# Optimization experiments

Hardware: AMD Instinct MI355X
Metric: run time of the kernel (lower is better)

## Reference

```python
import jax, jax.numpy as jnp
import numpy as np

N_ENT, N_REL, DIM, N_BASES = 100000, 474, 200, 100
N_EDGES, N_TRIPLES = 500000, 200000


def setup_inputs() -> dict:
    key = jax.random.key(0)
    ks = jax.random.split(key, 12)
    s = np.sqrt(2.0 / (1 + 0.01 ** 2))  # kaiming-ish scale (exact init irrelevant for correctness baseline)
    return {
        "entity_embeds": jax.random.normal(ks[0], (N_ENT, DIM), jnp.float32) * 0.05,
        "bases": jax.random.normal(ks[1], (N_BASES, DIM), jnp.float32) * 0.05,
        "coefficients": jax.random.normal(ks[2], (N_REL, N_BASES), jnp.float32) * 0.05,
        "w1": jax.random.normal(ks[3], (3, DIM, DIM), jnp.float32) * (s / np.sqrt(DIM)),
        "rw1": jax.random.normal(ks[4], (DIM, DIM), jnp.float32) * (s / np.sqrt(DIM)),
        "w2": jax.random.normal(ks[5], (3, DIM, DIM), jnp.float32) * (s / np.sqrt(DIM)),
        "rw2": jax.random.normal(ks[6], (DIM, DIM), jnp.float32) * (s / np.sqrt(DIM)),
        "ent_ids": jnp.arange(N_ENT, dtype=jnp.int32),
        "edge_index": jax.random.randint(ks[7], (2, N_EDGES), 0, N_ENT, jnp.int32),
        "edge_type": jax.random.randint(ks[8], (N_EDGES,), 0, N_REL, jnp.int32),
        "y": jax.random.randint(ks[9], (N_EDGES,), 0, 3, jnp.int32),
        "triples": jax.random.randint(ks[10], (N_TRIPLES, 3), 0, N_REL, jnp.int32),
    }


def _compgcn_layer(x, r, W, RW, edge_index, edge_type, y, n_nodes):
    # message: x_j + r[edge_type], then per-edge-direction linear transform W[y]
    msgs = x[edge_index[0]] + r[edge_type]            # [E, d]
    t = jnp.einsum('ed,kdf->kef', msgs, W)            # [3, E, d] (avoids [E,d,d] gather)
    sel = jnp.where(y[:, None] == 0, t[0], jnp.where(y[:, None] == 1, t[1], t[2]))  # [E, d]
    agg = jax.ops.segment_sum(sel, edge_index[1], num_segments=n_nodes)  # aggr='add'
    return jnp.tanh(agg), r @ RW


def reference(entity_embeds, bases, coefficients, w1, rw1, w2, rw2,
              ent_ids, edge_index, edge_type, y, triples):
    # encode (eval mode: dropout is identity)
    x = entity_embeds[ent_ids]
    r = coefficients @ bases                          # [num_relations, d]
    n_nodes = x.shape[0]
    x, r = _compgcn_layer(x, r, w1, rw1, edge_index, edge_type, y, n_nodes)
    x, r = _compgcn_layer(x, r, w2, rw2, edge_index, edge_type, y, n_nodes)
    # L2 normalize (torch eps=1e-12)
    x = x / jnp.maximum(jnp.linalg.norm(x, axis=1, keepdims=True), 1e-12)
    # decode: TransE-style L1 distance, sigmoid
    h = x[triples[:, 0]]
    rel = r[triples[:, 1]]
    t = x[triples[:, 2]]
    scores = jnp.sum(jnp.abs(h + rel - t), axis=1)    # norm p=1
    return jax.nn.sigmoid(scores)
```

## Files before the change

kernel.cpp:

```cpp
#include <hip/hip_runtime.h>
#include <math.h>


#define NENT     100000
#define NREL     474
#define DIM      200
#define NBASES   100
#define NEDGES   500000
#define NTRIPLES 200000

#define CHUNK    50000
#define NCHUNKS  2
#define SD       608
#define KD       608
#define NPAD     224
#define NTILW    7

#define OFF_R1    0UL
#define OFF_R2    380928UL
#define OFF_R3    761856UL
#define OFF_R1B   1142784UL
#define OFF_R2B   1335296UL
#define OFF_DEG   1527808UL
#define OFF_CUR   1929216UL
#define OFF_CSR   2330624UL
#define OFF_BSUM  2732032UL
#define OFF_BOFF  2736128UL
#define OFF_CSRC  2740224UL
#define OFF_CRY   4743168UL
#define OFF_WT1   6746112UL
#define OFF_WT2   7020544UL
#define OFF_ENTB  7294976UL
#define OFF_X1B   47296512UL
#define OFF_SBUF  87298048UL
#define OFF_X2    148099072UL

typedef __attribute__((ext_vector_type(8))) short bf16x8;
typedef __attribute__((ext_vector_type(4))) float f32x4;

__device__ inline unsigned short f2bf(float f) {
    unsigned u = __float_as_uint(f);
    return (unsigned short)((u + 0x7FFFu + ((u >> 16) & 1u)) >> 16);
}
__device__ inline float bf2f(unsigned short s) {
    return __uint_as_float(((unsigned)s) << 16);
}

__global__ __launch_bounds__(256) void k_small_gemm(
    const float* __restrict__ A, const float* __restrict__ B,
    float* __restrict__ C, int M, int K, int N)
{
    int tid = blockIdx.x * blockDim.x + threadIdx.x;
    if (tid >= M * N) return;
    int row = tid / N, col = tid - row * N;
    const float* a = A + (long)row * K;
    float acc = 0.f;
    int k = 0;
    for (; k + 4 <= K; k += 4) {
        acc = fmaf(a[k + 0], B[(k + 0) * N + col], acc);
        acc = fmaf(a[k + 1], B[(k + 1) * N + col], acc);
        acc = fmaf(a[k + 2], B[(k + 2) * N + col], acc);
        acc = fmaf(a[k + 3], B[(k + 3) * N + col], acc);
    }
    for (; k < K; ++k) acc = fmaf(a[k], B[k * N + col], acc);
    C[tid] = acc;
}

__global__ __launch_bounds__(256) void k_rb(const float* __restrict__ in,
                                            unsigned short* __restrict__ out, int n)
{
    int i = blockIdx.x * 256 + threadIdx.x;
    if (i < n) out[i] = f2bf(in[i]);
}

__global__ __launch_bounds__(256) void k_wt(const float* __restrict__ W,
                                            unsigned short* __restrict__ Wt)
{
    int i = blockIdx.x * 256 + threadIdx.x;
    if (i >= NPAD * KD) return;
    int c = i / KD, k = i - c * KD;
    float v = (c < 200 && k < 600) ? W[k * 200 + c] : 0.f;
    Wt[i] = f2bf(v);
}

__global__ __launch_bounds__(256) void k_entb(const float4* __restrict__ ent,
                                              const int* __restrict__ ids,
                                              ushort4* __restrict__ out)
{
    int i = blockIdx.x * 256 + threadIdx.x;
    if (i >= NENT * 50) return;
    int node = i / 50, j = i - node * 50;
    float4 v = ent[(long)ids[node] * 50 + j];
    ushort4 o;
    o.x = f2bf(v.x); o.y = f2bf(v.y); o.z = f2bf(v.z); o.w = f2bf(v.w);
    out[i] = o;
}

__global__ __launch_bounds__(256) void k_hist(const int* __restrict__ ei, int* __restrict__ deg)
{
    int e = blockIdx.x * blockDim.x + threadIdx.x;
    if (e >= NEDGES) return;
    atomicAdd(&deg[ei[NEDGES + e]], 1);
}

__global__ __launch_bounds__(256) void k_scanA(
    const int* __restrict__ deg, int* __restrict__ out, int* __restrict__ bsum)
{
    __shared__ int sd[256];
    int t = threadIdx.x, b = blockIdx.x;
    int base = b * 1024 + t * 4;
    int v0 = (base + 0 < NENT) ? deg[base + 0] : 0;
    int v1 = (base + 1 < NENT) ? deg[base + 1] : 0;
    int v2 = (base + 2 < NENT) ? deg[base + 2] : 0;
    int v3 = (base + 3 < NENT) ? deg[base + 3] : 0;
    int s = v0 + v1 + v2 + v3;
    sd[t] = s; __syncthreads();
    for (int off = 1; off < 256; off <<= 1) {
        int x = (t >= off) ? sd[t - off] : 0;
        __syncthreads();
        sd[t] += x;
        __syncthreads();
    }
    int excl = sd[t] - s;
    if (base + 0 < NENT) out[base + 0] = excl;
    if (base + 1 < NENT) out[base + 1] = excl + v0;
    if (base + 2 < NENT) out[base + 2] = excl + v0 + v1;
    if (base + 3 < NENT) out[base + 3] = excl + v0 + v1 + v2;
    if (t == 255) bsum[b] = sd[255];
}

__global__ __launch_bounds__(128) void k_scanB(
    const int* __restrict__ bsum, int* __restrict__ boff, int nb)
{
    __shared__ int sd[128];
    int t = threadIdx.x;
    int s = (t < nb) ? bsum[t] : 0;
    sd[t] = s; __syncthreads();
    for (int off = 1; off < 128; off <<= 1) {
        int x = (t >= off) ? sd[t - off] : 0;
        __syncthreads();
        sd[t] += x;
        __syncthreads();
    }
    if (t < nb) boff[t] = sd[t] - s;
}

__global__ __launch_bounds__(256) void k_scanC(int* __restrict__ csr, const int* __restrict__ boff)
{
    int t = threadIdx.x, b = blockIdx.x;
    int base = b * 1024 + t * 4;
    int add = boff[b];
    #pragma unroll
    for (int i = 0; i < 4; ++i)
        if (base + i < NENT) csr[base + i] += add;
    if (b == 0 && t == 0) csr[NENT] = NEDGES;
}

__global__ __launch_bounds__(256) void k_scatter(
    const int* __restrict__ ei, const int* __restrict__ et, const int* __restrict__ y,
    const int* __restrict__ csr, int* __restrict__ cur,
    int* __restrict__ csrc, int* __restrict__ cry)
{
    int e = blockIdx.x * blockDim.x + threadIdx.x;
    if (e >= NEDGES) return;
    int dst = ei[NEDGES + e];
    int pos = csr[dst] + atomicAdd(&cur[dst], 1);
    csrc[pos] = ei[e];
    cry[pos]  = et[e] | (y[e] << 16);
}

__global__ __launch_bounds__(256) void k_accum(
    const unsigned short* __restrict__ xb,
    const unsigned short* __restrict__ rb,
    const int* __restrict__ csr, const int* __restrict__ csrc, const int* __restrict__ cry,
    unsigned short* __restrict__ S, int nodeBase)
{
    int wv   = (blockIdx.x * blockDim.x + threadIdx.x) >> 6;
    int lane = threadIdx.x & 63;
    unsigned short* srow = S + (long)wv * SD;
    if (lane >= 50) {
        if (lane == 50) {
            uint4 z; z.x = z.y = z.z = z.w = 0u;
            *(uint4*)(srow + 600) = z;
        }
        return;
    }
    int v = nodeBase + wv;
    int start = csr[v], end = csr[v + 1];
    float4 a0 = {0,0,0,0}, a1 = {0,0,0,0}, a2 = {0,0,0,0};
    for (int e = start; e < end; ++e) {
        int src = csrc[e];
        int ry  = cry[e];
        int rel = ry & 0xFFFF;
        int k   = ry >> 16;
        ushort4 xv = *(const ushort4*)(xb + (long)src * 200 + lane * 4);
        ushort4 rv = *(const ushort4*)(rb + (long)rel * 200 + lane * 4);
        float mx = bf2f(xv.x) + bf2f(rv.x), my = bf2f(xv.y) + bf2f(rv.y);
        float mz = bf2f(xv.z) + bf2f(rv.z), mw = bf2f(xv.w) + bf2f(rv.w);
        if (k == 0)      { a0.x += mx; a0.y += my; a0.z += mz; a0.w += mw; }
        else if (k == 1) { a1.x += mx; a1.y += my; a1.z += mz; a1.w += mw; }
        else             { a2.x += mx; a2.y += my; a2.z += mz; a2.w += mw; }
    }
    ushort4 o;
    o.x = f2bf(a0.x); o.y = f2bf(a0.y); o.z = f2bf(a0.z); o.w = f2bf(a0.w);
    *(ushort4*)(srow +   0 + lane * 4) = o;
    o.x = f2bf(a1.x); o.y = f2bf(a1.y); o.z = f2bf(a1.z); o.w = f2bf(a1.w);
    *(ushort4*)(srow + 200 + lane * 4) = o;
    o.x = f2bf(a2.x); o.y = f2bf(a2.y); o.z = f2bf(a2.z); o.w = f2bf(a2.w);
    *(ushort4*)(srow + 400 + lane * 4) = o;
}

template<int OUTBF>
__global__ __launch_bounds__(256) void k_gemm_mfma(
    const unsigned short* __restrict__ S, const unsigned short* __restrict__ Wt,
    void* __restrict__ Xout, int nrows, int rowBase)
{
    int wid  = threadIdx.x >> 6;
    int lane = threadIdx.x & 63;
    int l15  = lane & 15;
    int l4   = lane >> 4;
    int row0 = blockIdx.x * 32 + (wid & 1) * 16;
    int nt0  = (wid >> 1) * NTILW;
    int ra = row0 + l15; if (ra >= nrows) ra = nrows - 1;
    const unsigned short* pa = S  + (long)ra * SD + l4 * 8;
    const unsigned short* pw = Wt + (long)(nt0 * 16 + l15) * KD + l4 * 8;

    f32x4 acc[NTILW] = {};
    for (int kt = 0; kt < 19; ++kt) {
        bf16x8 a = *(const bf16x8*)(pa + kt * 32);
        #pragma unroll
        for (int nt = 0; nt < NTILW; ++nt) {
            bf16x8 b = *(const bf16x8*)(pw + nt * 16 * KD + kt * 32);
            acc[nt] = __builtin_amdgcn_mfma_f32_16x16x32_bf16(a, b, acc[nt], 0, 0, 0);
        }
    }
    #pragma unroll
    for (int nt = 0; nt < NTILW; ++nt) {
        int col = (nt0 + nt) * 16 + l15;
        bool cok = (col < DIM);
        #pragma unroll
        for (int i = 0; i < 4; ++i) {
            int r = row0 + l4 * 4 + i;
            if (cok && r < nrows) {
                float v = tanhf(acc[nt][i]);
                if (OUTBF) ((unsigned short*)Xout)[(long)(rowBase + r) * DIM + col] = f2bf(v);
                else       ((float*)Xout)[(long)(rowBase + r) * DIM + col] = v;
            }
        }
    }
}

__global__ __launch_bounds__(256) void k_norm(float4* __restrict__ x)
{
    int wv   = (blockIdx.x * blockDim.x + threadIdx.x) >> 6;
    int lane = threadIdx.x & 63;
    float4 v = {0,0,0,0};
    if (lane < 50) v = x[(long)wv * 50 + lane];
    float ss = v.x*v.x + v.y*v.y + v.z*v.z + v.w*v.w;
    for (int off = 1; off < 64; off <<= 1) ss += __shfl_xor(ss, off);
    float scale = 1.f / fmaxf(sqrtf(ss), 1e-12f);
    if (lane < 50) {
        v.x *= scale; v.y *= scale; v.z *= scale; v.w *= scale;
        x[(long)wv * 50 + lane] = v;
    }
}

__global__ __launch_bounds__(256) void k_score(
    const float4* __restrict__ x, const float4* __restrict__ r,
    const int* __restrict__ tri, float* __restrict__ out)
{
    int wv   = (blockIdx.x * blockDim.x + threadIdx.x) >> 6;
    int lane = threadIdx.x & 63;
    if (wv >= NTRIPLES) return;
    int h = tri[wv * 3 + 0], rel = tri[wv * 3 + 1], t = tri[wv * 3 + 2];
    float p = 0.f;
    if (lane < 50) {
        float4 hv = x[(long)h * 50 + lane];
        float4 rv = r[(long)rel * 50 + lane];
        float4 tv = x[(long)t * 50 + lane];
        p = fabsf(hv.x + rv.x - tv.x) + fabsf(hv.y + rv.y - tv.y)
          + fabsf(hv.z + rv.z - tv.z) + fabsf(hv.w + rv.w - tv.w);
    }
    for (int off = 1; off < 64; off <<= 1) p += __shfl_xor(p, off);
    if (lane == 0) out[wv] = 1.f / (1.f + expf(-p));
}

extern "C" void kernel_launch(void* const* d_in, const int* in_sizes, int n_in,
                              void* d_out, int out_size, void* d_ws, size_t ws_size,
                              hipStream_t stream)
{
    const float* ent    = (const float*)d_in[0];
    const float* bases  = (const float*)d_in[1];
    const float* coeff  = (const float*)d_in[2];
    const float* w1     = (const float*)d_in[3];
    const float* rw1    = (const float*)d_in[4];
    const float* w2     = (const float*)d_in[5];
    const float* rw2    = (const float*)d_in[6];
    const int*   entids = (const int*)d_in[7];
    const int*   ei     = (const int*)d_in[8];
    const int*   etype  = (const int*)d_in[9];
    const int*   yv     = (const int*)d_in[10];
    const int*   tri    = (const int*)d_in[11];
    float* out = (float*)d_out;

    char* ws = (char*)d_ws;
    float* r1   = (float*)(ws + OFF_R1);
    float* r2   = (float*)(ws + OFF_R2);
    float* r3   = (float*)(ws + OFF_R3);
    unsigned short* r1b = (unsigned short*)(ws + OFF_R1B);
    unsigned short* r2b = (unsigned short*)(ws + OFF_R2B);
    int* deg    = (int*)(ws + OFF_DEG);
    int* cur    = (int*)(ws + OFF_CUR);
    int* csr    = (int*)(ws + OFF_CSR);
    int* bsum   = (int*)(ws + OFF_BSUM);
    int* boff   = (int*)(ws + OFF_BOFF);
    int* csrc   = (int*)(ws + OFF_CSRC);
    int* cry    = (int*)(ws + OFF_CRY);
    unsigned short* wt1  = (unsigned short*)(ws + OFF_WT1);
    unsigned short* wt2  = (unsigned short*)(ws + OFF_WT2);
    unsigned short* entb = (unsigned short*)(ws + OFF_ENTB);
    unsigned short* x1b  = (unsigned short*)(ws + OFF_X1B);
    unsigned short* Sbuf = (unsigned short*)(ws + OFF_SBUF);
    float* x2   = (float*)(ws + OFF_X2);

    hipMemsetAsync(ws + OFF_DEG, 0, OFF_CSR - OFF_DEG, stream);

    {
        int tot = NREL * DIM;
        int nb = (tot + 255) / 256;
        k_small_gemm<<<nb, 256, 0, stream>>>(coeff, bases, r1, NREL, NBASES, DIM);
        k_small_gemm<<<nb, 256, 0, stream>>>(r1, rw1, r2, NREL, DIM, DIM);
        k_small_gemm<<<nb, 256, 0, stream>>>(r2, rw2, r3, NREL, DIM, DIM);
        k_rb<<<nb, 256, 0, stream>>>(r1, r1b, tot);
        k_rb<<<nb, 256, 0, stream>>>(r2, r2b, tot);
    }

    k_wt<<<(NPAD * KD + 255) / 256, 256, 0, stream>>>(w1, wt1);
    k_wt<<<(NPAD * KD + 255) / 256, 256, 0, stream>>>(w2, wt2);
    k_entb<<<(NENT * 50 + 255) / 256, 256, 0, stream>>>(
        (const float4*)ent, entids, (ushort4*)entb);

    k_hist<<<(NEDGES + 255) / 256, 256, 0, stream>>>(ei, deg);
    int nScanBlocks = (NENT + 1023) / 1024;
    k_scanA<<<nScanBlocks, 256, 0, stream>>>(deg, csr, bsum);
    k_scanB<<<1, 128, 0, stream>>>(bsum, boff, nScanBlocks);
    k_scanC<<<nScanBlocks, 256, 0, stream>>>(csr, boff);
    k_scatter<<<(NEDGES + 255) / 256, 256, 0, stream>>>(ei, etype, yv, csr, cur, csrc, cry);

    int gblocks = (CHUNK + 31) / 32;

    for (int c = 0; c < NCHUNKS; ++c) {
        int base = c * CHUNK;
        k_accum<<<CHUNK * 64 / 256, 256, 0, stream>>>(entb, r1b,
                                                      csr, csrc, cry, Sbuf, base);
        k_gemm_mfma<1><<<gblocks, 256, 0, stream>>>(Sbuf, wt1, (void*)x1b, CHUNK, base);
    }
    for (int c = 0; c < NCHUNKS; ++c) {
        int base = c * CHUNK;
        k_accum<<<CHUNK * 64 / 256, 256, 0, stream>>>(x1b, r2b,
                                                      csr, csrc, cry, Sbuf, base);
        k_gemm_mfma<0><<<gblocks, 256, 0, stream>>>(Sbuf, wt2, (void*)x2, CHUNK, base);
    }

    k_norm<<<NENT / 4, 256, 0, stream>>>((float4*)x2);
    k_score<<<(NTRIPLES + 3) / 4, 256, 0, stream>>>(
        (const float4*)x2, (const float4*)r3, tri, out);
}
```

Measured before the change: 799.0 us.

## Retile MFMA GEMM to 2x4 register tiles with software-prefetched operands

Each wave in the MFMA GEMM now computes 32 rows by 64 columns (two A fragments times four B fragments) instead of 16 rows by 112 columns. Each loaded fragment is reused across more MFMAs, and the next k-step's operands are loaded before the current MFMAs are issued. The weight padding grows from 224 to 256 columns, with the buffer offsets shifted to match, so four waves cover the N dimension evenly. This wastes MFMA work on the padded columns 200-255, and `__launch_bounds__(256,4)` limits the registers available per thread.

```diff
diff --git a/kernel.cpp b/kernel.cpp
--- a/kernel.cpp
+++ b/kernel.cpp
@@ -13,8 +13,7 @@
 #define NCHUNKS  2
 #define SD       608
 #define KD       608
-#define NPAD     224
-#define NTILW    7
+#define NPAD     256
 
 #define OFF_R1    0UL
 #define OFF_R2    380928UL
@@ -29,11 +28,11 @@
 #define OFF_CSRC  2740224UL
 #define OFF_CRY   4743168UL
 #define OFF_WT1   6746112UL
-#define OFF_WT2   7020544UL
-#define OFF_ENTB  7294976UL
-#define OFF_X1B   47296512UL
-#define OFF_SBUF  87298048UL
-#define OFF_X2    148099072UL
+#define OFF_WT2   7057408UL
+#define OFF_ENTB  7368704UL
+#define OFF_X1B   47369216UL
+#define OFF_SBUF  87369728UL
+#define OFF_X2    148169728UL
 
 typedef __attribute__((ext_vector_type(8))) short bf16x8;
 typedef __attribute__((ext_vector_type(4))) float f32x4;
@@ -211,7 +210,7 @@
 }
 
 template<int OUTBF>
-__global__ __launch_bounds__(256) void k_gemm_mfma(
+__global__ __launch_bounds__(256, 4) void k_gemm_mfma(
     const unsigned short* __restrict__ S, const unsigned short* __restrict__ Wt,
     void* __restrict__ Xout, int nrows, int rowBase)
 {
@@ -219,32 +218,65 @@
     int lane = threadIdx.x & 63;
     int l15  = lane & 15;
     int l4   = lane >> 4;
-    int row0 = blockIdx.x * 32 + (wid & 1) * 16;
-    int nt0  = (wid >> 1) * NTILW;
-    int ra = row0 + l15; if (ra >= nrows) ra = nrows - 1;
-    const unsigned short* pa = S  + (long)ra * SD + l4 * 8;
-    const unsigned short* pw = Wt + (long)(nt0 * 16 + l15) * KD + l4 * 8;
-
-    f32x4 acc[NTILW] = {};
+    int row0 = blockIdx.x * 32;
+    int ra = row0 + l15;      if (ra >= nrows) ra = nrows - 1;
+    int rb = row0 + 16 + l15; if (rb >= nrows) rb = nrows - 1;
+    const unsigned short* pa0 = S  + (long)ra * SD + l4 * 8;
+    const unsigned short* pa1 = S  + (long)rb * SD + l4 * 8;
+    const unsigned short* pw  = Wt + (long)(wid * 64 + l15) * KD + l4 * 8;
+
+    bf16x8 a0c = *(const bf16x8*)(pa0);
+    bf16x8 a1c = *(const bf16x8*)(pa1);
+    bf16x8 bc0 = *(const bf16x8*)(pw + 0 * 16 * KD);
+    bf16x8 bc1 = *(const bf16x8*)(pw + 1 * 16 * KD);
+    bf16x8 bc2 = *(const bf16x8*)(pw + 2 * 16 * KD);
+    bf16x8 bc3 = *(const bf16x8*)(pw + 3 * 16 * KD);
+
+    f32x4 acc0[4] = {};
+    f32x4 acc1[4] = {};
+    #pragma unroll
     for (int kt = 0; kt < 19; ++kt) {
-        bf16x8 a = *(const bf16x8*)(pa + kt * 32);
-        #pragma unroll
-        for (int nt = 0; nt < NTILW; ++nt) {
-            bf16x8 b = *(const bf16x8*)(pw + nt * 16 * KD + kt * 32);
-            acc[nt] = __builtin_amdgcn_mfma_f32_16x16x32_bf16(a, b, acc[nt], 0, 0, 0);
+        bf16x8 a0n, a1n, bn0, bn1, bn2, bn3;
+        if (kt < 18) {
+            int o = (kt + 1) * 32;
+            a0n = *(const bf16x8*)(pa0 + o);
+            a1n = *(const bf16x8*)(pa1 + o);
+            bn0 = *(const bf16x8*)(pw + 0 * 16 * KD + o);
+            bn1 = *(const bf16x8*)(pw + 1 * 16 * KD + o);
+            bn2 = *(const bf16x8*)(pw + 2 * 16 * KD + o);
+            bn3 = *(const bf16x8*)(pw + 3 * 16 * KD + o);
         }
-    }
+        acc0[0] = __builtin_amdgcn_mfma_f32_16x16x32_bf16(a0c, bc0, acc0[0], 0, 0, 0);
+        acc1[0] = __builtin_amdgcn_mfma_f32_16x16x32_bf16(a1c, bc0, acc1[0], 0, 0, 0);
+        acc0[1] = __builtin_amdgcn_mfma_f32_16x16x32_bf16(a0c, bc1, acc0[1], 0, 0, 0);
+        acc1[1] = __builtin_amdgcn_mfma_f32_16x16x32_bf16(a1c, bc1, acc1[1], 0, 0, 0);
+        acc0[2] = __builtin_amdgcn_mfma_f32_16x16x32_bf16(a0c, bc2, acc0[2], 0, 0, 0);
+        acc1[2] = __builtin_amdgcn_mfma_f32_16x16x32_bf16(a1c, bc2, acc1[2], 0, 0, 0);
+        acc0[3] = __builtin_amdgcn_mfma_f32_16x16x32_bf16(a0c, bc3, acc0[3], 0, 0, 0);
+        acc1[3] = __builtin_amdgcn_mfma_f32_16x16x32_bf16(a1c, bc3, acc1[3], 0, 0, 0);
+        if (kt < 18) {
+            a0c = a0n; a1c = a1n;
+            bc0 = bn0; bc1 = bn1; bc2 = bn2; bc3 = bn3;
+        }
+    }
+
     #pragma unroll
-    for (int nt = 0; nt < NTILW; ++nt) {
-        int col = (nt0 + nt) * 16 + l15;
+    for (int nt = 0; nt < 4; ++nt) {
+        int col = (wid * 4 + nt) * 16 + l15;
         bool cok = (col < DIM);
         #pragma unroll
         for (int i = 0; i < 4; ++i) {
-            int r = row0 + l4 * 4 + i;
-            if (cok && r < nrows) {
-                float v = tanhf(acc[nt][i]);
-                if (OUTBF) ((unsigned short*)Xout)[(long)(rowBase + r) * DIM + col] = f2bf(v);
-                else       ((float*)Xout)[(long)(rowBase + r) * DIM + col] = v;
+            int r0 = row0 + l4 * 4 + i;
+            if (cok && r0 < nrows) {
+                float v = tanhf(acc0[nt][i]);
+                if (OUTBF) ((unsigned short*)Xout)[(long)(rowBase + r0) * DIM + col] = f2bf(v);
+                else       ((float*)Xout)[(long)(rowBase + r0) * DIM + col] = v;
+            }
+            int r1 = r0 + 16;
+            if (cok && r1 < nrows) {
+                float v = tanhf(acc1[nt][i]);
+                if (OUTBF) ((unsigned short*)Xout)[(long)(rowBase + r1) * DIM + col] = f2bf(v);
+                else       ((float*)Xout)[(long)(rowBase + r1) * DIM + col] = v;
             }
         }
     }
```

New measurement: 743.3 us. 1.08x faster.

## Retile MFMA GEMM to 64-row blocks with 4x4 register tiles per wave

Applied to the files above, without the earlier changes.

The dense GEMM after neighbour accumulation now gives each block 64 rows, and each wave computes a 64x64 output tile as a 4x4 grid of 16x16 MFMA accumulators. W is padded to 256 columns so four waves cover the output columns. The aim is to reuse each loaded A and B fragment across four MFMAs, cutting global/L2 load traffic per MFMA compared with the old one-A, seven-B layout. Side changes are nontemporal loads for the streamed S rows and launch_bounds(256,2). The cost is more accumulator registers and some wasted MFMA work on the padded columns between 200 and 256.

```diff
diff --git a/kernel.cpp b/kernel.cpp
--- a/kernel.cpp
+++ b/kernel.cpp
@@ -13,8 +13,7 @@
 #define NCHUNKS  2
 #define SD       608
 #define KD       608
-#define NPAD     224
-#define NTILW    7
+#define NPAD     256
 
 #define OFF_R1    0UL
 #define OFF_R2    380928UL
@@ -29,11 +28,11 @@
 #define OFF_CSRC  2740224UL
 #define OFF_CRY   4743168UL
 #define OFF_WT1   6746112UL
-#define OFF_WT2   7020544UL
-#define OFF_ENTB  7294976UL
-#define OFF_X1B   47296512UL
-#define OFF_SBUF  87298048UL
-#define OFF_X2    148099072UL
+#define OFF_WT2   7057408UL
+#define OFF_ENTB  7368704UL
+#define OFF_X1B   47369216UL
+#define OFF_SBUF  87369728UL
+#define OFF_X2    148169728UL
 
 typedef __attribute__((ext_vector_type(8))) short bf16x8;
 typedef __attribute__((ext_vector_type(4))) float f32x4;
@@ -211,7 +210,7 @@
 }
 
 template<int OUTBF>
-__global__ __launch_bounds__(256) void k_gemm_mfma(
+__global__ __launch_bounds__(256, 2) void k_gemm_mfma(
     const unsigned short* __restrict__ S, const unsigned short* __restrict__ Wt,
     void* __restrict__ Xout, int nrows, int rowBase)
 {
@@ -219,32 +218,61 @@
     int lane = threadIdx.x & 63;
     int l15  = lane & 15;
     int l4   = lane >> 4;
-    int row0 = blockIdx.x * 32 + (wid & 1) * 16;
-    int nt0  = (wid >> 1) * NTILW;
-    int ra = row0 + l15; if (ra >= nrows) ra = nrows - 1;
-    const unsigned short* pa = S  + (long)ra * SD + l4 * 8;
-    const unsigned short* pw = Wt + (long)(nt0 * 16 + l15) * KD + l4 * 8;
-
-    f32x4 acc[NTILW] = {};
+    int row0 = blockIdx.x * 64;
+
+    const unsigned short* pa[4];
+    #pragma unroll
+    for (int rf = 0; rf < 4; ++rf) {
+        int r = row0 + rf * 16 + l15;
+        if (r >= nrows) r = nrows - 1;
+        pa[rf] = S + (long)r * SD + l4 * 8;
+    }
+    const unsigned short* pw = Wt + (long)(wid * 64 + l15) * KD + l4 * 8;
+
+    f32x4 acc[4][4] = {};
+    #pragma unroll 1
     for (int kt = 0; kt < 19; ++kt) {
-        bf16x8 a = *(const bf16x8*)(pa + kt * 32);
+        int o = kt * 32;
+        bf16x8 a0 = __builtin_nontemporal_load((const bf16x8*)(pa[0] + o));
+        bf16x8 a1 = __builtin_nontemporal_load((const bf16x8*)(pa[1] + o));
+        bf16x8 a2 = __builtin_nontemporal_load((const bf16x8*)(pa[2] + o));
+        bf16x8 a3 = __builtin_nontemporal_load((const bf16x8*)(pa[3] + o));
+        bf16x8 b0 = *(const bf16x8*)(pw + 0 * 16 * KD + o);
+        bf16x8 b1 = *(const bf16x8*)(pw + 1 * 16 * KD + o);
+        bf16x8 b2 = *(const bf16x8*)(pw + 2 * 16 * KD + o);
+        bf16x8 b3 = *(const bf16x8*)(pw + 3 * 16 * KD + o);
+        acc[0][0] = __builtin_amdgcn_mfma_f32_16x16x32_bf16(a0, b0, acc[0][0], 0, 0, 0);
+        acc[1][0] = __builtin_amdgcn_mfma_f32_16x16x32_bf16(a1, b0, acc[1][0], 0, 0, 0);
+        acc[2][0] = __builtin_amdgcn_mfma_f32_16x16x32_bf16(a2, b0, acc[2][0], 0, 0, 0);
+        acc[3][0] = __builtin_amdgcn_mfma_f32_16x16x32_bf16(a3, b0, acc[3][0], 0, 0, 0);
+        acc[0][1] = __builtin_amdgcn_mfma_f32_16x16x32_bf16(a0, b1, acc[0][1], 0, 0, 0);
+        acc[1][1] = __builtin_amdgcn_mfma_f32_16x16x32_bf16(a1, b1, acc[1][1], 0, 0, 0);
+        acc[2][1] = __builtin_amdgcn_mfma_f32_16x16x32_bf16(a2, b1, acc[2][1], 0, 0, 0);
+        acc[3][1] = __builtin_amdgcn_mfma_f32_16x16x32_bf16(a3, b1, acc[3][1], 0, 0, 0);
+        acc[0][2] = __builtin_amdgcn_mfma_f32_16x16x32_bf16(a0, b2, acc[0][2], 0, 0, 0);
+        acc[1][2] = __builtin_amdgcn_mfma_f32_16x16x32_bf16(a1, b2, acc[1][2], 0, 0, 0);
+        acc[2][2] = __builtin_amdgcn_mfma_f32_16x16x32_bf16(a2, b2, acc[2][2], 0, 0, 0);
+        acc[3][2] = __builtin_amdgcn_mfma_f32_16x16x32_bf16(a3, b2, acc[3][2], 0, 0, 0);
+        acc[0][3] = __builtin_amdgcn_mfma_f32_16x16x32_bf16(a0, b3, acc[0][3], 0, 0, 0);
+        acc[1][3] = __builtin_amdgcn_mfma_f32_16x16x32_bf16(a1, b3, acc[1][3], 0, 0, 0);
+        acc[2][3] = __builtin_amdgcn_mfma_f32_16x16x32_bf16(a2, b3, acc[2][3], 0, 0, 0);
+        acc[3][3] = __builtin_amdgcn_mfma_f32_16x16x32_bf16(a3, b3, acc[3][3], 0, 0, 0);
+    }
+
+    #pragma unroll
+    for (int rf = 0; rf < 4; ++rf) {
         #pragma unroll
-        for (int nt = 0; nt < NTILW; ++nt) {
-            bf16x8 b = *(const bf16x8*)(pw + nt * 16 * KD + kt * 32);
-            acc[nt] = __builtin_amdgcn_mfma_f32_16x16x32_bf16(a, b, acc[nt], 0, 0, 0);
-        }
-    }
-    #pragma unroll
-    for (int nt = 0; nt < NTILW; ++nt) {
-        int col = (nt0 + nt) * 16 + l15;
-        bool cok = (col < DIM);
-        #pragma unroll
-        for (int i = 0; i < 4; ++i) {
-            int r = row0 + l4 * 4 + i;
-            if (cok && r < nrows) {
-                float v = tanhf(acc[nt][i]);
-                if (OUTBF) ((unsigned short*)Xout)[(long)(rowBase + r) * DIM + col] = f2bf(v);
-                else       ((float*)Xout)[(long)(rowBase + r) * DIM + col] = v;
+        for (int nt = 0; nt < 4; ++nt) {
+            int col = (wid * 4 + nt) * 16 + l15;
+            bool cok = (col < DIM);
+            #pragma unroll
+            for (int i = 0; i < 4; ++i) {
+                int r = row0 + rf * 16 + l4 * 4 + i;
+                if (cok && r < nrows) {
+                    float v = tanhf(acc[rf][nt][i]);
+                    if (OUTBF) ((unsigned short*)Xout)[(long)(rowBase + r) * DIM + col] = f2bf(v);
+                    else       ((float*)Xout)[(long)(rowBase + r) * DIM + col] = v;
+                }
             }
         }
     }
@@ -347,7 +375,7 @@
     k_scanC<<<nScanBlocks, 256, 0, stream>>>(csr, boff);
     k_scatter<<<(NEDGES + 255) / 256, 256, 0, stream>>>(ei, etype, yv, csr, cur, csrc, cry);
 
-    int gblocks = (CHUNK + 31) / 32;
+    int gblocks = (CHUNK + 63) / 64;
 
     for (int c = 0; c < NCHUNKS; ++c) {
         int base = c * CHUNK;
```

Result: slower. 889.5 us (+11.3%).
